# Optimization experiments

Hardware: AMD Instinct MI355X
Metric: run time of the kernel (lower is better)

## Reference

```python
import jax, jax.numpy as jnp
import numpy as np

B, S, H, E, V, T, OOV = 32, 400, 256, 300, 50000, 20, 50


def setup_inputs() -> dict:
    key = jax.random.key(0)
    ks = jax.random.split(key, 24)
    g = lambda k, sh, scale=0.02: jax.random.normal(k, sh, dtype=jnp.float32) * scale
    return {
        "enc_hidden": jax.random.normal(ks[0], (B, S, 2 * H), dtype=jnp.float32),
        "h0": jax.random.normal(ks[1], (B, H), dtype=jnp.float32),
        "c0": jax.random.normal(ks[2], (B, H), dtype=jnp.float32),
        "embedding": g(ks[3], (V, E), 1.0),
        "W_enc": g(ks[4], (2 * H, H)),
        "W_dec": g(ks[5], (H, H)),
        "w_cov": g(ks[6], (H,)),
        "v_attn": g(ks[7], (H,)),
        "W_ih": g(ks[8], (E, 4 * H)),
        "W_hh": g(ks[9], (H, 4 * H)),
        "b_lstm": jnp.zeros((4 * H,), jnp.float32),
        "W_out1": g(ks[10], (3 * H, H)),
        "b_out1": jnp.zeros((H,), jnp.float32),
        "W_out2": g(ks[11], (H, V)),
        "b_out2": jnp.zeros((V,), jnp.float32),
        "w_h": g(ks[12], (2 * H, 1)),
        "w_s": g(ks[13], (H, 1)),
        "w_x": g(ks[14], (E, 1)),
        "b_x": jnp.zeros((1,), jnp.float32),
        "dec_input": jax.random.randint(ks[15], (B, T), 0, V),
        "enc_input_ext": jax.random.randint(ks[16], (B, S), 0, V + OOV),
        "enc_pad_mask": jnp.ones((B, S), dtype=bool),
        "max_oov_len": OOV,
    }


def reference(enc_hidden, h0, c0, embedding, W_enc, W_dec, w_cov, v_attn,
              W_ih, W_hh, b_lstm, W_out1, b_out1, W_out2, b_out2,
              w_h, w_s, w_x, b_x, dec_input, enc_input_ext, enc_pad_mask,
              max_oov_len):
    b, s, two_h = enc_hidden.shape
    enc_feat = enc_hidden @ W_enc  # [B,S,H], precomputed attention keys
    batch_idx = jnp.arange(b)[:, None]
    NEG = jnp.float32(-1e9)

    def step(carry, x_t):
        h, c, cov = carry
        emb = embedding[x_t]  # [B,E]
        # LSTM cell
        gates = emb @ W_ih + h @ W_hh + b_lstm
        i, f, gg, o = jnp.split(gates, 4, axis=-1)
        c = jax.nn.sigmoid(f) * c + jax.nn.sigmoid(i) * jnp.tanh(gg)
        h = jax.nn.sigmoid(o) * jnp.tanh(c)
        # coverage attention over encoder states
        e = jnp.tanh(enc_feat + (h @ W_dec)[:, None, :] + cov[..., None] * w_cov) @ v_attn  # [B,S]
        e = jnp.where(enc_pad_mask, e, NEG)
        attn = jax.nn.softmax(e, axis=-1)
        context = jnp.einsum('bs,bsd->bd', attn, enc_hidden)  # [B,2H]
        cov = cov + attn
        # vocab distribution
        out = jnp.concatenate([h, context], axis=-1) @ W_out1 + b_out1
        vocab_dist = jax.nn.softmax(out @ W_out2 + b_out2, axis=-1)  # [B,V]
        # pointer-generator gate
        p_gen = jax.nn.sigmoid(context @ w_h + h @ w_s + emb @ w_x + b_x)  # [B,1]
        vocab_dist = p_gen * vocab_dist
        weighted_attn = (1.0 - p_gen) * attn
        # extend vocab and scatter-add copy probabilities
        ext = jnp.concatenate(
            [vocab_dist, jnp.zeros((b, max_oov_len), vocab_dist.dtype)], axis=-1)
        final = ext.at[batch_idx, enc_input_ext].add(weighted_attn)
        return (h, c, cov), (final, attn, cov)

    cov0 = jnp.zeros((b, s), jnp.float32)
    _, (finals, attns, covs) = jax.lax.scan(step, (h0, c0, cov0), dec_input.T)
    # stack with time on the last axis, as in the torch module
    return (jnp.moveaxis(finals, 0, -1),
            jnp.moveaxis(attns, 0, -1),
            jnp.moveaxis(covs, 0, -1))
```

## Files before the change

### kernel.cpp

```cpp
#include <hip/hip_runtime.h>
#include <hip/hip_bf16.h>

#define B_    32
#define S_    400
#define H_    256
#define E_    300
#define V_    50000
#define T_    20
#define VE_   50050
#define TB_   640
#define VPAD_ 50048
#define FIN_  32032000
#define NB_   16
#define SC_   25

typedef __attribute__((ext_vector_type(8))) short bf16x8;
typedef __attribute__((ext_vector_type(4))) float f32x4;

__device__ __forceinline__ float sigmoid_f(float x){ return 1.f/(1.f+__expf(-x)); }
__device__ __forceinline__ float tanh_f(float x){ return 1.f - 2.f/(__expf(2.f*x)+1.f); }

__device__ __forceinline__ float bf2f(unsigned short u){
  union { unsigned int i; float f; } x; x.i = ((unsigned int)u) << 16; return x.f;
}
__device__ __forceinline__ unsigned short f2bf(float f){
  union { __hip_bfloat16 h; unsigned short u; } x; x.h = __float2bfloat16(f); return x.u;
}

__device__ __forceinline__ void st_dev(float* p, float v){
  __hip_atomic_store(p, v, __ATOMIC_RELAXED, __HIP_MEMORY_SCOPE_AGENT);
}
__device__ __forceinline__ float ld_dev(const float* p){
  return __hip_atomic_load(p, __ATOMIC_RELAXED, __HIP_MEMORY_SCOPE_AGENT);
}
__device__ __forceinline__ int ld_cnt(const int* p){
  return __hip_atomic_load(p, __ATOMIC_RELAXED, __HIP_MEMORY_SCOPE_AGENT);
}
__device__ __forceinline__ void add_cnt(int* p){
  __hip_atomic_fetch_add(p, 1, __ATOMIC_RELAXED, __HIP_MEMORY_SCOPE_AGENT);
}


__global__ __launch_bounds__(256) void kT(const float* __restrict__ in,
                                          __hip_bfloat16* __restrict__ out, int R, int C){
  __shared__ float tile[32][33];
  int tx = threadIdx.x & 31, ty = threadIdx.x >> 5;
  int c = blockIdx.x*32 + tx;
  #pragma unroll
  for (int i = 0; i < 4; ++i){
    int r = blockIdx.y*32 + ty + i*8;
    if (r < R && c < C) tile[ty + i*8][tx] = in[(size_t)r*C + c];
  }
  __syncthreads();
  int r2 = blockIdx.y*32 + tx;
  #pragma unroll
  for (int i = 0; i < 4; ++i){
    int c2 = blockIdx.x*32 + ty + i*8;
    if (r2 < R && c2 < C) out[(size_t)c2*R + r2] = __float2bfloat16(tile[tx][ty + i*8]);
  }
}

__global__ __launch_bounds__(256) void kpair2(const float* __restrict__ Whh,
                                              const float* __restrict__ Wdec,
                                              unsigned short* __restrict__ oW,
                                              unsigned short* __restrict__ oD){
  int g = blockIdx.x*256 + threadIdx.x;
  if (g < 262144){
    int k = g >> 10, n = g & 1023;
    oW[(size_t)(k >> 1)*2048 + n*2 + (k & 1)] = f2bf(Whh[g]);
  } else {
    int g2 = g - 262144;
    int k = g2 >> 8, n = g2 & 255;
    oD[(size_t)(k >> 1)*512 + n*2 + (k & 1)] = f2bf(Wdec[g2]);
  }
}

__global__ __launch_bounds__(256) void k1s(const float* __restrict__ emb,
                                           const int* __restrict__ dec,
                                           const float* __restrict__ W_ih,
                                           const float* __restrict__ b_lstm,
                                           float* __restrict__ pre_ih){
  int m = blockIdx.x;
  int r0 = m*2, r1 = m*2 + 1;
  int tid = threadIdx.x;
  __shared__ float e0[304], e1[304];
  int g0 = dec[(r0 & 31)*20 + (r0 >> 5)];
  int g1 = dec[(r1 & 31)*20 + (r1 >> 5)];
  for (int k = tid; k < 300; k += 256){
    e0[k] = emb[(size_t)g0*300 + k];
    e1[k] = emb[(size_t)g1*300 + k];
  }
  __syncthreads();
  float a0[4] = {}, a1[4] = {};
  #pragma unroll 4
  for (int k = 0; k < 300; ++k){
    const float* wr = W_ih + (size_t)k*1024 + tid;
    float w0 = wr[0], w1 = wr[256], w2 = wr[512], w3 = wr[768];
    float x0 = e0[k], x1 = e1[k];
    a0[0] += x0*w0; a0[1] += x0*w1; a0[2] += x0*w2; a0[3] += x0*w3;
    a1[0] += x1*w0; a1[1] += x1*w1; a1[2] += x1*w2; a1[3] += x1*w3;
  }
  #pragma unroll
  for (int j = 0; j < 4; ++j){
    float bl = b_lstm[tid + j*256];
    pre_ih[(size_t)r0*1024 + tid + j*256] = a0[j] + bl;
    pre_ih[(size_t)r1*1024 + tid + j*256] = a1[j] + bl;
  }
}

__global__ __launch_bounds__(256) void k2(const float* __restrict__ EH,
                                          const __hip_bfloat16* __restrict__ Bt,
                                          __hip_bfloat16* __restrict__ Cbf){
  int tid = threadIdx.x;
  int lane = tid & 63, wave = tid >> 6;
  int wm = wave >> 1, wn = wave & 1;
  int n0 = blockIdx.x*128, m0 = blockIdx.y*128;
  __shared__ __align__(16) unsigned short A_s[128][40];
  __shared__ __align__(16) unsigned short B_s[128][40];
  f32x4 acc[4][4];
  #pragma unroll
  for (int i = 0; i < 4; ++i)
    #pragma unroll
    for (int j = 0; j < 4; ++j) acc[i][j] = (f32x4){0.f,0.f,0.f,0.f};
  int cg = tid & 3;
  for (int kc = 0; kc < 16; ++kc){
    __syncthreads();
    #pragma unroll
    for (int rr = 0; rr < 2; ++rr){
      int row = (tid >> 2) + rr*64;
      const float* src = EH + (size_t)(m0+row)*512 + kc*32 + cg*8;
      float4 f0 = *(const float4*)src;
      float4 f1 = *(const float4*)(src + 4);
      unsigned int u0 = ((unsigned int)f2bf(f0.y) << 16) | f2bf(f0.x);
      unsigned int u1 = ((unsigned int)f2bf(f0.w) << 16) | f2bf(f0.z);
      unsigned int u2 = ((unsigned int)f2bf(f1.y) << 16) | f2bf(f1.x);
      unsigned int u3 = ((unsigned int)f2bf(f1.w) << 16) | f2bf(f1.z);
      unsigned int* dst = (unsigned int*)&A_s[row][cg*8];
      dst[0] = u0; dst[1] = u1; dst[2] = u2; dst[3] = u3;
      *(float4*)&B_s[row][cg*8] = *(const float4*)(Bt + (size_t)(n0+row)*512 + kc*32 + cg*8);
    }
    __syncthreads();
    bf16x8 af[4], bfr[4];
    #pragma unroll
    for (int mt = 0; mt < 4; ++mt)
      af[mt] = *(const bf16x8*)&A_s[wm*64 + mt*16 + (lane & 15)][(lane >> 4)*8];
    #pragma unroll
    for (int nt = 0; nt < 4; ++nt)
      bfr[nt] = *(const bf16x8*)&B_s[wn*64 + nt*16 + (lane & 15)][(lane >> 4)*8];
    #pragma unroll
    for (int mt = 0; mt < 4; ++mt)
      #pragma unroll
      for (int nt = 0; nt < 4; ++nt)
        acc[mt][nt] = __builtin_amdgcn_mfma_f32_16x16x32_bf16(af[mt], bfr[nt], acc[mt][nt], 0, 0, 0);
  }
  int lm = lane & 15, lq = lane >> 4;
  #pragma unroll
  for (int mt = 0; mt < 4; ++mt)
    #pragma unroll
    for (int nt = 0; nt < 4; ++nt){
      int vv = n0 + wn*64 + nt*16 + lm;
      #pragma unroll
      for (int rg = 0; rg < 4; ++rg){
        int r = m0 + wm*64 + mt*16 + lq*4 + rg;
        Cbf[(size_t)r*256 + vv] = __float2bfloat16(acc[mt][nt][rg]);
      }
    }
}

__global__ __launch_bounds__(256) void krec(
    const float* __restrict__ h0, const float* __restrict__ c0,
    const unsigned short* __restrict__ Whh2,
    const unsigned short* __restrict__ Wd2,
    const float* __restrict__ w_cov, const float* __restrict__ v_attn,
    const float* __restrict__ pre_ih, const __hip_bfloat16* __restrict__ enc_feat,
    const float* __restrict__ enc_hidden,
    float* __restrict__ H_all, float* __restrict__ exps_g,
    float* __restrict__ Zatt, float* __restrict__ ctxp,
    float* __restrict__ hdecp, int* bar)
{
  const int bx = blockIdx.x;
  const int b = (bx & 7) + 8*((bx >> 3) & 3);
  const int jj = bx >> 5;
  const int tid = threadIdx.x;
  const int lane = tid & 63, wave = tid >> 6;
  const int s0 = jj*SC_;

  __shared__ __align__(16) unsigned short eh_s[SC_][512];
  __shared__ __align__(16) unsigned short ef_s[SC_][256];
  __shared__ float h_pad[272];
  __shared__ float hdec_sh[256], vat[256], wcv[256];
  __shared__ float h_loc[16];
  __shared__ float covf[32], ehist[2][32];
  __shared__ float invZ_sh;

  for (int e = tid; e < SC_*128; e += 256){
    int row = e >> 7, c4 = e & 127;
    float4 f = *(const float4*)(enc_hidden + ((size_t)(b*400 + s0 + row))*512 + c4*4);
    unsigned int lo = ((unsigned int)f2bf(f.y) << 16) | f2bf(f.x);
    unsigned int hi = ((unsigned int)f2bf(f.w) << 16) | f2bf(f.z);
    *(unsigned int*)&eh_s[row][c4*4]     = lo;
    *(unsigned int*)&eh_s[row][c4*4 + 2] = hi;
  }
  for (int e = tid; e < SC_*32; e += 256){
    int row = e >> 5, c8 = e & 31;
    *(float4*)&ef_s[row][c8*8] =
      *(const float4*)(enc_feat + ((size_t)(b*400 + s0 + row))*256 + c8*8);
  }
  vat[tid] = v_attn[tid];
  wcv[tid] = w_cov[tid];
  h_pad[tid + 4*(tid >> 6)] = h0[b*256 + tid];
  if (tid < 32) covf[tid] = 0.f;

  const int kq = lane & 3, cl = (lane >> 2) & 3, gt = lane >> 4;
  const int ci = wave*4 + cl;
  const int gcol = gt*256 + jj*16 + ci;
  ushort2 wreg[32];
  #pragma unroll
  for (int pp = 0; pp < 32; ++pp)
    wreg[pp] = *(const ushort2*)(Whh2 + ((size_t)(kq*32 + pp))*2048 + gcol*2);
  ushort2 wdreg[8];
  #pragma unroll
  for (int p = 0; p < 8; ++p)
    wdreg[p] = *(const ushort2*)(Wd2 + ((size_t)(jj*8 + p))*512 + tid*2);
  float c_reg = c0[b*256 + jj*16 + ci];

  __syncthreads();

  int* cnt_h = bar + b*16;
  int* cnt_z = cnt_h + 4;

  {
    float acc = (kq == 0) ? pre_ih[(size_t)b*1024 + gcol] : 0.f;
    const float* hb = &h_pad[kq*68];
    #pragma unroll
    for (int pp = 0; pp < 32; ++pp){
      float2 h2 = *(const float2*)&hb[pp*2];
      acc += h2.x*bf2f(wreg[pp].x) + h2.y*bf2f(wreg[pp].y);
    }
    acc += __shfl_xor(acc, 1);
    acc += __shfl_xor(acc, 2);
    int base = lane & 12;
    float gi = __shfl(acc, base);
    float gf = __shfl(acc, base + 16);
    float gG = __shfl(acc, base + 32);
    float go = __shfl(acc, base + 48);
    float cn = sigmoid_f(gf)*c_reg + sigmoid_f(gi)*tanh_f(gG);
    c_reg = cn;
    float hv = sigmoid_f(go)*tanh_f(cn);
    if ((lane & 51) == 0){
      st_dev(&H_all[(size_t)b*256 + jj*16 + ci], hv);
      h_loc[ci] = hv;
    }
  }
  __syncthreads();
  {
    float pd = 0.f;
    #pragma unroll
    for (int p = 0; p < 8; ++p)
      pd += h_loc[p*2]*bf2f(wdreg[p].x) + h_loc[p*2 + 1]*bf2f(wdreg[p].y);
    st_dev(&hdecp[((size_t)b*16 + jj)*256 + tid], pd);
  }
  __syncthreads();
  if (tid == 0) add_cnt(cnt_h);

  #pragma unroll 1
  for (int t = 0; t < T_; ++t){
    const int r = t*32 + b;
    float pihn = (kq == 0 && t < T_-1) ? pre_ih[(size_t)(r+32)*1024 + gcol] : 0.f;
    if (tid == 0){
      while (ld_cnt(cnt_h) < NB_*(t + 1)) __builtin_amdgcn_s_sleep(1);
    }
    __syncthreads();
    {
      float hfull = ld_dev(&H_all[(size_t)r*256 + tid]);
      float hd = 0.f;
      #pragma unroll
      for (int j2 = 0; j2 < 16; ++j2)
        hd += ld_dev(&hdecp[((size_t)r*16 + j2)*256 + tid]);
      h_pad[tid + 4*(tid >> 6)] = hfull;
      hdec_sh[tid] = hd;
    }
    __syncthreads();
    if (t < T_-1){
      float acc = pihn;
      const float* hb = &h_pad[kq*68];
      #pragma unroll
      for (int pp = 0; pp < 32; ++pp){
        float2 h2 = *(const float2*)&hb[pp*2];
        acc += h2.x*bf2f(wreg[pp].x) + h2.y*bf2f(wreg[pp].y);
      }
      acc += __shfl_xor(acc, 1);
      acc += __shfl_xor(acc, 2);
      int base = lane & 12;
      float gi = __shfl(acc, base);
      float gf = __shfl(acc, base + 16);
      float gG = __shfl(acc, base + 32);
      float go = __shfl(acc, base + 48);
      float cn = sigmoid_f(gf)*c_reg + sigmoid_f(gi)*tanh_f(gG);
      c_reg = cn;
      float hv = sigmoid_f(go)*tanh_f(cn);
      if ((lane & 51) == 0){
        st_dev(&H_all[(size_t)(r+32)*256 + jj*16 + ci], hv);
        h_loc[ci] = hv;
      }
    }
    __syncthreads();
    if (t < T_-1){
      float pd = 0.f;
      #pragma unroll
      for (int p = 0; p < 8; ++p)
        pd += h_loc[p*2]*bf2f(wdreg[p].x) + h_loc[p*2 + 1]*bf2f(wdreg[p].y);
      st_dev(&hdecp[((size_t)(r+32)*16 + jj)*256 + tid], pd);
    }
    __syncthreads();
    if (tid == 0){
      if (t < T_-1) add_cnt(cnt_h);
      if (t > 0){
        while (ld_cnt(cnt_z) < NB_*t) __builtin_amdgcn_s_sleep(1);
        invZ_sh = 1.f/ld_dev(&Zatt[r - 32]);
      }
    }
    __syncthreads();
    float* ecur = ehist[t & 1];
    const float* eprev = ehist[(t ^ 1) & 1];
    float invz = invZ_sh;
    for (int sl = wave; sl < SC_; sl += 4){
      float cw = covf[sl];
      if (t > 0) cw += eprev[sl]*invz;
      float part = 0.f;
      #pragma unroll
      for (int q = 0; q < 4; ++q){
        int k = lane + q*64;
        float x = bf2f(ef_s[sl][k]) + hdec_sh[k] + cw*wcv[k];
        part += vat[k]*tanh_f(x);
      }
      #pragma unroll
      for (int off = 32; off > 0; off >>= 1) part += __shfl_xor(part, off);
      if (lane == 0){
        covf[sl] = cw;
        float ev = __expf(part);
        ecur[sl] = ev;
        exps_g[(size_t)r*400 + s0 + sl] = ev;
      }
    }
    __syncthreads();
    if (tid == 0){
      float z = 0.f;
      #pragma unroll
      for (int q = 0; q < SC_; ++q) z += ecur[q];
      atomicAdd(&Zatt[r], z);
      asm volatile("s_waitcnt vmcnt(0)" ::: "memory");
      add_cnt(cnt_z);
    }
    #pragma unroll
    for (int hh = 0; hh < 2; ++hh){
      int d = tid + hh*256;
      float a2 = 0.f;
      #pragma unroll
      for (int sl = 0; sl < SC_; ++sl) a2 += ecur[sl]*bf2f(eh_s[sl][d]);
      ctxp[((size_t)r*16 + jj)*512 + d] = a2;
    }
  }
}

__global__ __launch_bounds__(256) void k3a(const float* __restrict__ Zatt,
                                           const float* __restrict__ ctxp,
                                           const float* __restrict__ H_all,
                                           const float* __restrict__ w_h,
                                           const float* __restrict__ w_s,
                                           const float* __restrict__ emb,
                                           const int* __restrict__ dec,
                                           const float* __restrict__ w_x,
                                           const float* __restrict__ b_x,
                                           float* __restrict__ CAT,
                                           float* __restrict__ pgen){
  int r = blockIdx.x, tid = threadIdx.x;
  __shared__ float red[256];
  float invz = 1.f/Zatt[r];
  float hv = H_all[(size_t)r*256 + tid];
  CAT[(size_t)r*768 + tid] = hv;
  float a0 = 0.f, a1 = 0.f;
  const float* p = ctxp + (size_t)r*16*512;
  #pragma unroll
  for (int jj = 0; jj < 16; ++jj){
    a0 += p[jj*512 + tid];
    a1 += p[jj*512 + 256 + tid];
  }
  float cv0 = a0*invz;
  float cv1 = a1*invz;
  CAT[(size_t)r*768 + 256 + tid] = cv0;
  CAT[(size_t)r*768 + 512 + tid] = cv1;
  int gid = dec[(r & 31)*20 + (r >> 5)];
  float px = 0.f;
  for (int k = tid; k < 300; k += 256) px += emb[(size_t)gid*300 + k]*w_x[k];
  float pg = hv*w_s[tid] + cv0*w_h[tid] + cv1*w_h[tid + 256];
  red[tid] = pg + px; __syncthreads();
  for (int st = 128; st > 0; st >>= 1){
    if (tid < st) red[tid] += red[tid + st];
    __syncthreads();
  }
  if (tid == 0) pgen[r] = sigmoid_f(red[0] + b_x[0]);
}

__global__ __launch_bounds__(256) void k3b(const float* __restrict__ exps_g,
                                           const float* __restrict__ Zatt,
                                           float* __restrict__ attns,
                                           float* __restrict__ covs){
  __shared__ float tA[256*20];
  __shared__ float tC[256*20];
  int tid = threadIdx.x;
  int g0 = blockIdx.x*256;
  int g = g0 + tid;
  int b = g / 400, s = g % 400;
  float cum = 0.f;
  for (int t = 0; t < T_; ++t){
    int r = t*32 + b;
    float a = exps_g[(size_t)r*400 + s] / Zatt[r];
    cum += a;
    tA[tid*20 + t] = a;
    tC[tid*20 + t] = cum;
  }
  __syncthreads();
  size_t base = (size_t)g0*20;
  for (int e = tid; e < 5120; e += 256){
    attns[base + e] = tA[e];
    covs[base + e]  = tC[e];
  }
}

__global__ __launch_bounds__(256) void k4(const float* __restrict__ CAT,
                                          const float* __restrict__ W_out1,
                                          const float* __restrict__ b_out1,
                                          __hip_bfloat16* __restrict__ OUTb){
  int tid = threadIdx.x;
  int n0 = blockIdx.x*64, m0 = blockIdx.y*64;
  __shared__ float A_s[64][17];
  __shared__ float B_s[16][65];
  float acc[4][4] = {};
  int ty = tid >> 4, tx = tid & 15;
  for (int kc = 0; kc < 48; ++kc){
    __syncthreads();
    for (int e = tid; e < 1024; e += 256){
      int row = e >> 4, kk = e & 15;
      A_s[row][kk] = CAT[(size_t)(m0 + row)*768 + kc*16 + kk];
    }
    for (int e = tid; e < 1024; e += 256){
      int kk = e >> 6, c = e & 63;
      B_s[kk][c] = W_out1[(size_t)(kc*16 + kk)*256 + n0 + c];
    }
    __syncthreads();
    #pragma unroll
    for (int kk = 0; kk < 16; ++kk){
      float av[4], bv[4];
      #pragma unroll
      for (int i = 0; i < 4; ++i) av[i] = A_s[ty*4 + i][kk];
      #pragma unroll
      for (int j = 0; j < 4; ++j) bv[j] = B_s[kk][tx*4 + j];
      #pragma unroll
      for (int i = 0; i < 4; ++i)
        #pragma unroll
        for (int j = 0; j < 4; ++j) acc[i][j] += av[i]*bv[j];
    }
  }
  #pragma unroll
  for (int i = 0; i < 4; ++i)
    #pragma unroll
    for (int j = 0; j < 4; ++j){
      int rr = m0 + ty*4 + i, cc = n0 + tx*4 + j;
      OUTb[(size_t)rr*256 + cc] = __float2bfloat16(acc[i][j] + b_out1[cc]);
    }
}

__global__ __launch_bounds__(256) void k5(const __hip_bfloat16* __restrict__ OUTb,
                                          const __hip_bfloat16* __restrict__ W2t,
                                          const float* __restrict__ b_out2,
                                          __hip_bfloat16* __restrict__ temp,
                                          float* __restrict__ Zsum){
  int tid = threadIdx.x;
  int lane = tid & 63, wave = tid >> 6;
  int wm = wave >> 1, wn = wave & 1;
  int n0 = blockIdx.y*128, m0 = blockIdx.x*128;
  __shared__ __align__(16) unsigned short A_s[128][40];
  __shared__ __align__(16) unsigned short B_s[128][40];
  f32x4 acc[4][4];
  #pragma unroll
  for (int i = 0; i < 4; ++i)
    #pragma unroll
    for (int j = 0; j < 4; ++j) acc[i][j] = (f32x4){0.f,0.f,0.f,0.f};
  int cg = tid & 3;
  for (int kc = 0; kc < 8; ++kc){
    __syncthreads();
    #pragma unroll
    for (int rr = 0; rr < 2; ++rr){
      int row = (tid >> 2) + rr*64;
      *(float4*)&A_s[row][cg*8] = *(const float4*)(OUTb + (size_t)(m0 + row)*256 + kc*32 + cg*8);
      int v = n0 + row;
      float4 bv = make_float4(0.f, 0.f, 0.f, 0.f);
      if (v < V_) bv = *(const float4*)(W2t + (size_t)v*256 + kc*32 + cg*8);
      *(float4*)&B_s[row][cg*8] = bv;
    }
    __syncthreads();
    bf16x8 af[4], bfr[4];
    #pragma unroll
    for (int mt = 0; mt < 4; ++mt)
      af[mt] = *(const bf16x8*)&A_s[wm*64 + mt*16 + (lane & 15)][(lane >> 4)*8];
    #pragma unroll
    for (int nt = 0; nt < 4; ++nt)
      bfr[nt] = *(const bf16x8*)&B_s[wn*64 + nt*16 + (lane & 15)][(lane >> 4)*8];
    #pragma unroll
    for (int mt = 0; mt < 4; ++mt)
      #pragma unroll
      for (int nt = 0; nt < 4; ++nt)
        acc[mt][nt] = __builtin_amdgcn_mfma_f32_16x16x32_bf16(af[mt], bfr[nt], acc[mt][nt], 0, 0, 0);
  }
  int lm = lane & 15, lq = lane >> 4;
  float rowsum[4][4];
  #pragma unroll
  for (int mt = 0; mt < 4; ++mt)
    #pragma unroll
    for (int rg = 0; rg < 4; ++rg) rowsum[mt][rg] = 0.f;
  #pragma unroll
  for (int mt = 0; mt < 4; ++mt)
    #pragma unroll
    for (int nt = 0; nt < 4; ++nt){
      int vv = n0 + wn*64 + nt*16 + lm;
      float b2 = (vv < V_) ? b_out2[vv] : 0.f;
      #pragma unroll
      for (int rg = 0; rg < 4; ++rg){
        int r = m0 + wm*64 + mt*16 + lq*4 + rg;
        float e = __expf(acc[mt][nt][rg] + b2);
        temp[(size_t)r*VPAD_ + vv] = __float2bfloat16(e);
        if (vv >= V_) e = 0.f;
        rowsum[mt][rg] += e;
      }
    }
  #pragma unroll
  for (int mt = 0; mt < 4; ++mt)
    #pragma unroll
    for (int rg = 0; rg < 4; ++rg){
      float s = rowsum[mt][rg];
      s += __shfl_xor(s, 1); s += __shfl_xor(s, 2);
      s += __shfl_xor(s, 4); s += __shfl_xor(s, 8);
      if (lm == 0){
        int r = m0 + wm*64 + mt*16 + lq*4 + rg;
        atomicAdd(&Zsum[r], s);
      }
    }
}

__global__ __launch_bounds__(256) void k6(const __hip_bfloat16* __restrict__ temp,
                                          const float* __restrict__ pgen,
                                          const float* __restrict__ Zsum,
                                          float* __restrict__ finals){
  int b = blockIdx.y, cb = blockIdx.x, tid = threadIdx.x;
  int v0 = cb*512;
  __shared__ float tile[20][513];
  __shared__ float ssc[20];
  if (tid < 20){ int r = tid*32 + b; ssc[tid] = pgen[r]/Zsum[r]; }
  __syncthreads();
  for (int e = tid; e < 1280; e += 256){
    int tt = e >> 6, c8 = e & 63;
    int v = v0 + c8*8;
    float sc = ssc[tt];
    const __hip_bfloat16* src = temp + (size_t)(tt*32 + b)*VPAD_ + v;
    if (v + 7 < V_){
      float4 raw = *(const float4*)src;
      const unsigned short* u = (const unsigned short*)&raw;
      #pragma unroll
      for (int j = 0; j < 8; ++j) tile[tt][c8*8 + j] = bf2f(u[j])*sc;
    } else {
      #pragma unroll
      for (int j = 0; j < 8; ++j)
        tile[tt][c8*8 + j] = (v + j < V_) ? __bfloat162float(src[j])*sc : 0.f;
    }
  }
  __syncthreads();
  int wlim = (VE_ - v0)*20; if (wlim > 10240) wlim = 10240;
  float* dst = finals + (size_t)b*1001000 + (size_t)v0*20;
  for (int e = tid; e < wlim; e += 256){
    dst[e] = tile[e % 20][e / 20];
  }
}

__global__ __launch_bounds__(320) void k7(const float* __restrict__ exps_g,
                                          const float* __restrict__ Zatt,
                                          const float* __restrict__ pgen,
                                          const int* __restrict__ ext,
                                          float* __restrict__ finals){
  int tid = threadIdx.x;
  int g = blockIdx.x*16 + tid/20;
  int t = tid % 20;
  int b = g / 400, s = g % 400;
  int r = t*32 + b;
  int idx = ext[g];
  float w = (1.f - pgen[r])*exps_g[(size_t)r*400 + s]/Zatt[r];
  atomicAdd(finals + (size_t)b*1001000 + (size_t)idx*20 + t, w);
}

extern "C" void kernel_launch(void* const* d_in, const int* in_sizes, int n_in,
                              void* d_out, int out_size, void* d_ws, size_t ws_size,
                              hipStream_t stream){
  const float* enc_hidden = (const float*)d_in[0];
  const float* h0         = (const float*)d_in[1];
  const float* c0         = (const float*)d_in[2];
  const float* embedding  = (const float*)d_in[3];
  const float* W_enc      = (const float*)d_in[4];
  const float* W_dec      = (const float*)d_in[5];
  const float* w_cov      = (const float*)d_in[6];
  const float* v_attn     = (const float*)d_in[7];
  const float* W_ih       = (const float*)d_in[8];
  const float* W_hh       = (const float*)d_in[9];
  const float* b_lstm     = (const float*)d_in[10];
  const float* W_out1     = (const float*)d_in[11];
  const float* b_out1     = (const float*)d_in[12];
  const float* W_out2     = (const float*)d_in[13];
  const float* b_out2     = (const float*)d_in[14];
  const float* w_h        = (const float*)d_in[15];
  const float* w_s        = (const float*)d_in[16];
  const float* w_x        = (const float*)d_in[17];
  const float* b_x        = (const float*)d_in[18];
  const int*   dec_input  = (const int*)d_in[19];
  const int*   enc_ext    = (const int*)d_in[20];

  float* out    = (float*)d_out;
  float* finals = out;
  float* attns  = out + FIN_;
  float* covs   = out + FIN_ + 256000;

  char* w = (char*)d_ws;
  auto alloc = [&](size_t n){ char* p = w; w += (n + 255) & ~(size_t)255; return p; };
  int*   bar      = (int*)  alloc(32*64);
  float* Zsum     = (float*)alloc((size_t)TB_*4);
  float* Zatt     = (float*)alloc((size_t)TB_*4);
  float* pre_ih   = (float*)alloc((size_t)TB_*1024*4);
  unsigned short* Whh2 = (unsigned short*)alloc((size_t)256*1024*2);
  unsigned short* Wd2  = (unsigned short*)alloc((size_t)256*256*2);
  __hip_bfloat16* WencT    = (__hip_bfloat16*)alloc((size_t)256*512*2);
  __hip_bfloat16* W2t      = (__hip_bfloat16*)alloc((size_t)V_*256*2);
  __hip_bfloat16* enc_feat = (__hip_bfloat16*)alloc((size_t)12800*256*2);
  float* H_all    = (float*)alloc((size_t)TB_*256*4);
  float* exps_g   = (float*)alloc((size_t)TB_*400*4);
  float* CAT      = (float*)alloc((size_t)TB_*768*4);
  float* pgen     = (float*)alloc((size_t)TB_*4);
  __hip_bfloat16* OUTb = (__hip_bfloat16*)alloc((size_t)TB_*256*2);
  __hip_bfloat16* temp = (__hip_bfloat16*)alloc((size_t)TB_*VPAD_*2);
  float* ctxp     = (float*)temp;
  float* hdecp    = (float*)((char*)temp + (size_t)TB_*16*512*4);

  hipMemsetAsync(bar, 0, 32*64, stream);
  hipMemsetAsync(Zsum, 0, (size_t)TB_*4, stream);
  hipMemsetAsync(Zatt, 0, (size_t)TB_*4, stream);

  kT <<<dim3(8, 16), 256, 0, stream>>>(W_enc, WencT, 512, 256);
  kT <<<dim3(1563, 8), 256, 0, stream>>>(W_out2, W2t, 256, V_);
  kpair2<<<1280, 256, 0, stream>>>(W_hh, W_dec, Whh2, Wd2);
  k1s<<<320, 256, 0, stream>>>(embedding, dec_input, W_ih, b_lstm, pre_ih);
  k2 <<<dim3(2, 100), 256, 0, stream>>>(enc_hidden, WencT, enc_feat);
  krec<<<512, 256, 0, stream>>>(h0, c0, Whh2, Wd2, w_cov, v_attn, pre_ih,
                                enc_feat, enc_hidden,
                                H_all, exps_g, Zatt, ctxp, hdecp, bar);
  k3a<<<640, 256, 0, stream>>>(Zatt, ctxp, H_all, w_h, w_s,
                               embedding, dec_input, w_x, b_x, CAT, pgen);
  k3b<<<50, 256, 0, stream>>>(exps_g, Zatt, attns, covs);
  k4 <<<dim3(4, 10), 256, 0, stream>>>(CAT, W_out1, b_out1, OUTb);
  k5 <<<dim3(5, 391), 256, 0, stream>>>(OUTb, W2t, b_out2, temp, Zsum);
  k6 <<<dim3(98, 32), 256, 0, stream>>>(temp, pgen, Zsum, finals);
  k7 <<<800, 320, 0, stream>>>(exps_g, Zatt, pgen, enc_ext, finals);
}
```

Before: 826.0 us.

## Persist A tile across vocab tiles in k5 and simplify the out1 GEMM

Result: faster. 793.4 us (-3.9%).

```diff
diff --git a/kernel.cpp b/kernel.cpp
--- a/kernel.cpp
+++ b/kernel.cpp
@@ -13,6 +13,7 @@
 #define FIN_  32032000
 #define NB_   16
 #define SC_   25
+#define K5NT  8
 
 typedef __attribute__((ext_vector_type(8))) short bf16x8;
 typedef __attribute__((ext_vector_type(4))) float f32x4;
@@ -428,47 +429,28 @@
   }
 }
 
-__global__ __launch_bounds__(256) void k4(const float* __restrict__ CAT,
-                                          const float* __restrict__ W_out1,
-                                          const float* __restrict__ b_out1,
-                                          __hip_bfloat16* __restrict__ OUTb){
-  int tid = threadIdx.x;
-  int n0 = blockIdx.x*64, m0 = blockIdx.y*64;
-  __shared__ float A_s[64][17];
-  __shared__ float B_s[16][65];
-  float acc[4][4] = {};
-  int ty = tid >> 4, tx = tid & 15;
-  for (int kc = 0; kc < 48; ++kc){
-    __syncthreads();
-    for (int e = tid; e < 1024; e += 256){
-      int row = e >> 4, kk = e & 15;
-      A_s[row][kk] = CAT[(size_t)(m0 + row)*768 + kc*16 + kk];
-    }
-    for (int e = tid; e < 1024; e += 256){
-      int kk = e >> 6, c = e & 63;
-      B_s[kk][c] = W_out1[(size_t)(kc*16 + kk)*256 + n0 + c];
-    }
-    __syncthreads();
-    #pragma unroll
-    for (int kk = 0; kk < 16; ++kk){
-      float av[4], bv[4];
-      #pragma unroll
-      for (int i = 0; i < 4; ++i) av[i] = A_s[ty*4 + i][kk];
-      #pragma unroll
-      for (int j = 0; j < 4; ++j) bv[j] = B_s[kk][tx*4 + j];
-      #pragma unroll
-      for (int i = 0; i < 4; ++i)
-        #pragma unroll
-        for (int j = 0; j < 4; ++j) acc[i][j] += av[i]*bv[j];
-    }
-  }
-  #pragma unroll
-  for (int i = 0; i < 4; ++i)
-    #pragma unroll
-    for (int j = 0; j < 4; ++j){
-      int rr = m0 + ty*4 + i, cc = n0 + tx*4 + j;
-      OUTb[(size_t)rr*256 + cc] = __float2bfloat16(acc[i][j] + b_out1[cc]);
-    }
+__global__ __launch_bounds__(256) void k4s(const float* __restrict__ CAT,
+                                           const float* __restrict__ W1,
+                                           const float* __restrict__ b1,
+                                           __hip_bfloat16* __restrict__ OUTb){
+  int m = blockIdx.x, tid = threadIdx.x;
+  int r0 = m*2, r1 = r0 + 1;
+  __shared__ float c0s[768], c1s[768];
+  for (int k = tid; k < 768; k += 256){
+    c0s[k] = CAT[(size_t)r0*768 + k];
+    c1s[k] = CAT[(size_t)r1*768 + k];
+  }
+  __syncthreads();
+  float a0 = 0.f, a1 = 0.f;
+  #pragma unroll 4
+  for (int k = 0; k < 768; ++k){
+    float w = W1[(size_t)k*256 + tid];
+    a0 += c0s[k]*w;
+    a1 += c1s[k]*w;
+  }
+  float bb = b1[tid];
+  OUTb[(size_t)r0*256 + tid] = __float2bfloat16(a0 + bb);
+  OUTb[(size_t)r1*256 + tid] = __float2bfloat16(a1 + bb);
 }
 
 __global__ __launch_bounds__(256) void k5(const __hip_bfloat16* __restrict__ OUTb,
@@ -479,73 +461,81 @@
   int tid = threadIdx.x;
   int lane = tid & 63, wave = tid >> 6;
   int wm = wave >> 1, wn = wave & 1;
-  int n0 = blockIdx.y*128, m0 = blockIdx.x*128;
-  __shared__ __align__(16) unsigned short A_s[128][40];
-  __shared__ __align__(16) unsigned short B_s[128][40];
-  f32x4 acc[4][4];
-  #pragma unroll
-  for (int i = 0; i < 4; ++i)
-    #pragma unroll
-    for (int j = 0; j < 4; ++j) acc[i][j] = (f32x4){0.f,0.f,0.f,0.f};
-  int cg = tid & 3;
-  for (int kc = 0; kc < 8; ++kc){
-    __syncthreads();
-    #pragma unroll
-    for (int rr = 0; rr < 2; ++rr){
-      int row = (tid >> 2) + rr*64;
-      *(float4*)&A_s[row][cg*8] = *(const float4*)(OUTb + (size_t)(m0 + row)*256 + kc*32 + cg*8);
+  int m0 = blockIdx.x*128;
+  int ng = blockIdx.y;
+  __shared__ __align__(16) unsigned short A_s[128][264];
+  __shared__ __align__(16) unsigned short B_s[128][264];
+  for (int e = tid; e < 4096; e += 256){
+    int row = e >> 5, c8 = e & 31;
+    *(float4*)&A_s[row][c8*8] = *(const float4*)(OUTb + (size_t)(m0 + row)*256 + c8*8);
+  }
+  int lm = lane & 15, lq = lane >> 4;
+  #pragma unroll 1
+  for (int ti = 0; ti < K5NT; ++ti){
+    int n0 = (ng*K5NT + ti)*128;
+    if (n0 >= VPAD_) break;
+    __syncthreads();
+    for (int e = tid; e < 4096; e += 256){
+      int row = e >> 5, c8 = e & 31;
       int v = n0 + row;
       float4 bv = make_float4(0.f, 0.f, 0.f, 0.f);
-      if (v < V_) bv = *(const float4*)(W2t + (size_t)v*256 + kc*32 + cg*8);
-      *(float4*)&B_s[row][cg*8] = bv;
-    }
-    __syncthreads();
-    bf16x8 af[4], bfr[4];
+      if (v < V_) bv = *(const float4*)(W2t + (size_t)v*256 + c8*8);
+      *(float4*)&B_s[row][c8*8] = bv;
+    }
+    __syncthreads();
+    f32x4 acc[4][4];
+    #pragma unroll
+    for (int i = 0; i < 4; ++i)
+      #pragma unroll
+      for (int j = 0; j < 4; ++j) acc[i][j] = (f32x4){0.f,0.f,0.f,0.f};
+    #pragma unroll
+    for (int ks = 0; ks < 8; ++ks){
+      bf16x8 af[4], bfr[4];
+      #pragma unroll
+      for (int mt = 0; mt < 4; ++mt)
+        af[mt] = *(const bf16x8*)&A_s[wm*64 + mt*16 + lm][lq*8 + ks*32];
+      #pragma unroll
+      for (int nt = 0; nt < 4; ++nt)
+        bfr[nt] = *(const bf16x8*)&B_s[wn*64 + nt*16 + lm][lq*8 + ks*32];
+      #pragma unroll
+      for (int mt = 0; mt < 4; ++mt)
+        #pragma unroll
+        for (int nt = 0; nt < 4; ++nt)
+          acc[mt][nt] = __builtin_amdgcn_mfma_f32_16x16x32_bf16(af[mt], bfr[nt], acc[mt][nt], 0, 0, 0);
+    }
+    float rowsum[4][4];
     #pragma unroll
     for (int mt = 0; mt < 4; ++mt)
-      af[mt] = *(const bf16x8*)&A_s[wm*64 + mt*16 + (lane & 15)][(lane >> 4)*8];
-    #pragma unroll
-    for (int nt = 0; nt < 4; ++nt)
-      bfr[nt] = *(const bf16x8*)&B_s[wn*64 + nt*16 + (lane & 15)][(lane >> 4)*8];
+      #pragma unroll
+      for (int rg = 0; rg < 4; ++rg) rowsum[mt][rg] = 0.f;
     #pragma unroll
     for (int mt = 0; mt < 4; ++mt)
       #pragma unroll
-      for (int nt = 0; nt < 4; ++nt)
-        acc[mt][nt] = __builtin_amdgcn_mfma_f32_16x16x32_bf16(af[mt], bfr[nt], acc[mt][nt], 0, 0, 0);
-  }
-  int lm = lane & 15, lq = lane >> 4;
-  float rowsum[4][4];
-  #pragma unroll
-  for (int mt = 0; mt < 4; ++mt)
-    #pragma unroll
-    for (int rg = 0; rg < 4; ++rg) rowsum[mt][rg] = 0.f;
-  #pragma unroll
-  for (int mt = 0; mt < 4; ++mt)
-    #pragma unroll
-    for (int nt = 0; nt < 4; ++nt){
-      int vv = n0 + wn*64 + nt*16 + lm;
-      float b2 = (vv < V_) ? b_out2[vv] : 0.f;
+      for (int nt = 0; nt < 4; ++nt){
+        int vv = n0 + wn*64 + nt*16 + lm;
+        float b2 = (vv < V_) ? b_out2[vv] : 0.f;
+        #pragma unroll
+        for (int rg = 0; rg < 4; ++rg){
+          int r = m0 + wm*64 + mt*16 + lq*4 + rg;
+          float e = __expf(acc[mt][nt][rg] + b2);
+          temp[(size_t)r*VPAD_ + vv] = __float2bfloat16(e);
+          if (vv >= V_) e = 0.f;
+          rowsum[mt][rg] += e;
+        }
+      }
+    #pragma unroll
+    for (int mt = 0; mt < 4; ++mt)
       #pragma unroll
       for (int rg = 0; rg < 4; ++rg){
-        int r = m0 + wm*64 + mt*16 + lq*4 + rg;
-        float e = __expf(acc[mt][nt][rg] + b2);
-        temp[(size_t)r*VPAD_ + vv] = __float2bfloat16(e);
-        if (vv >= V_) e = 0.f;
-        rowsum[mt][rg] += e;
-      }
-    }
-  #pragma unroll
-  for (int mt = 0; mt < 4; ++mt)
-    #pragma unroll
-    for (int rg = 0; rg < 4; ++rg){
-      float s = rowsum[mt][rg];
-      s += __shfl_xor(s, 1); s += __shfl_xor(s, 2);
-      s += __shfl_xor(s, 4); s += __shfl_xor(s, 8);
-      if (lm == 0){
-        int r = m0 + wm*64 + mt*16 + lq*4 + rg;
-        atomicAdd(&Zsum[r], s);
-      }
-    }
+        float s = rowsum[mt][rg];
+        s += __shfl_xor(s, 1); s += __shfl_xor(s, 2);
+        s += __shfl_xor(s, 4); s += __shfl_xor(s, 8);
+        if (lm == 0){
+          int r = m0 + wm*64 + mt*16 + lq*4 + rg;
+          atomicAdd(&Zsum[r], s);
+        }
+      }
+  }
 }
 
 __global__ __launch_bounds__(256) void k6(const __hip_bfloat16* __restrict__ temp,
@@ -662,8 +652,8 @@
   k3a<<<640, 256, 0, stream>>>(Zatt, ctxp, H_all, w_h, w_s,
                                embedding, dec_input, w_x, b_x, CAT, pgen);
   k3b<<<50, 256, 0, stream>>>(exps_g, Zatt, attns, covs);
-  k4 <<<dim3(4, 10), 256, 0, stream>>>(CAT, W_out1, b_out1, OUTb);
-  k5 <<<dim3(5, 391), 256, 0, stream>>>(OUTb, W2t, b_out2, temp, Zsum);
+  k4s<<<320, 256, 0, stream>>>(CAT, W_out1, b_out1, OUTb);
+  k5 <<<dim3(5, 49), 256, 0, stream>>>(OUTb, W2t, b_out2, temp, Zsum);
   k6 <<<dim3(98, 32), 256, 0, stream>>>(temp, pgen, Zsum, finals);
   k7 <<<800, 320, 0, stream>>>(exps_g, Zatt, pgen, enc_ext, finals);
 }
```
